# Kernel optimization log

Measured on AMD Instinct MI355X. Metric: run time of the kernel, lower is better.

The kernel has to match this reference:

```python
import jax, jax.numpy as jnp
import numpy as np

IN_F, OUT_F = 4096, 14336
F8_MAX = 448.0  # max magnitude of float8_e4m3fn


def setup_inputs() -> dict:
    key = jax.random.key(0)
    kx, kw, kb = jax.random.split(key, 3)
    x = jax.random.normal(kx, (2, 512, IN_F), dtype=jnp.bfloat16)
    w = jax.random.normal(kw, (OUT_F, IN_F), dtype=jnp.float32) * 0.02
    # per-tensor scale: amax / 448 (as in F8Linear.__init__)
    w_scale = (jnp.maximum(jnp.abs(w).max(), 1e-30) / F8_MAX).astype(jnp.float32)
    # quantize to fp8 e4m3; roundtrip back to float32 so the stored values are
    # exactly the fp8-representable values (float32 container keeps the bwd
    # reference's jax.vjp happy while the math is identical)
    w_f8 = jnp.clip(w / w_scale, -F8_MAX, F8_MAX).astype(jnp.float8_e4m3fn).astype(jnp.float32)
    bias = jax.random.normal(kb, (OUT_F,), dtype=jnp.float32) * 0.02
    return {"x": x, "weight_f8": w_f8, "w_scale": w_scale, "bias": bias}


def reference(x, weight_f8, w_scale, bias):
    # dequantize to activation dtype, then GEMM: y = x @ w^T + b
    w = weight_f8.astype(x.dtype) * w_scale.astype(x.dtype)   # [out, in]
    y = jnp.einsum('bsi,oi->bso', x, w) + bias.astype(x.dtype)
    return y
```

## Files before the change

### kernel.cpp

```cpp
#include <hip/hip_runtime.h>
#include <hip/hip_bf16.h>
#include <stdint.h>


#define IN_F   4096
#define OUT_F  14336
#define M_TOT  1024

#define BM 128
#define BN 128

#define TM 256
#define TN 256
#define TK 64
#define KT8 (IN_F / TK)

typedef __bf16  bf16x8 __attribute__((ext_vector_type(8)));
typedef __bf16  bf16x4 __attribute__((ext_vector_type(4)));
typedef float   f32x4  __attribute__((ext_vector_type(4)));

__device__ __forceinline__ void async_copy16(const void* g, void* l) {
    __builtin_amdgcn_global_load_lds(
        (const __attribute__((address_space(1))) void*)g,
        (__attribute__((address_space(3))) void*)l,
        16, 0, 0);
}

__global__ void detect_x_dtype(const uint32_t* __restrict__ xb,
                               int* __restrict__ flag) {
    __shared__ int any_low;
    if (threadIdx.x == 0) any_low = 0;
    __syncthreads();
    uint32_t bad = 0;
    for (int i = threadIdx.x; i < 1024; i += 256) bad |= (xb[i] & 0xFFFFu);
    if (bad) atomicOr(&any_low, 1);
    __syncthreads();
    if (threadIdx.x == 0) *flag = (any_low == 0) ? 1 : 0;
}

__global__ __launch_bounds__(256) void cvt_x_kernel(
    const void* __restrict__ xraw, bf16x8* __restrict__ out,
    const int* __restrict__ flag) {
    const int f32w = (*flag != 0);
    const int i = blockIdx.x * 256 + threadIdx.x;
    if (f32w) {
        const f32x4* in = (const f32x4*)xraw;
        f32x4 a = in[2 * i];
        f32x4 b = in[2 * i + 1];
        bf16x8 o;
        o[0] = (__bf16)a[0]; o[1] = (__bf16)a[1];
        o[2] = (__bf16)a[2]; o[3] = (__bf16)a[3];
        o[4] = (__bf16)b[0]; o[5] = (__bf16)b[1];
        o[6] = (__bf16)b[2]; o[7] = (__bf16)b[3];
        out[i] = o;
    } else {
        out[i] = ((const bf16x8*)xraw)[i];
    }
}

__global__ __launch_bounds__(512, 2) void gemm_fused_1b(
    const __bf16* __restrict__ xb,
    const float*  __restrict__ wf,
    const float*  __restrict__ w_scale,
    const float*  __restrict__ bias,
    void*         __restrict__ yraw,
    const int*    __restrict__ flag_p)
{
    __shared__ __align__(16) __bf16 As[2][2][128 * TK];
    __shared__ __align__(16) __bf16 Bs[2][2][128 * TK];

    const int f32w = (*flag_p != 0);
    const int t    = threadIdx.x;
    const int lane = t & 63;
    const int wv   = t >> 6;
    const int wm   = wv >> 2;
    const int wn   = wv & 3;
    const int lidx = lane & 15;
    const int q    = lane >> 4;

    const int flat = blockIdx.x;
    const int xcd  = flat & 7;
    const int slot = flat >> 3;
    const int ni   = xcd * 7 + (slot >> 2);
    const int mi   = slot & 3;
    const int m0   = mi * TM;
    const int n0   = ni * TN;

    const float scale = w_scale[0];

    const __bf16* gA = xb + (size_t)m0 * IN_F;

    int srow[2], scgl[2];
    #pragma unroll
    for (int i = 0; i < 2; ++i) {
        const int s = i * 512 + t;
        srow[i] = s >> 3;
        scgl[i] = (s & 7) ^ (srow[i] & 7);
    }

    const float* gB0 = wf + (size_t)(n0 + srow[0]) * IN_F + scgl[0] * 8;
    const float* gB1 = wf + (size_t)(n0 + srow[1]) * IN_F + scgl[1] * 8;

    int aoff[4][2], boff[2][2];
    #pragma unroll
    for (int qm = 0; qm < 4; ++qm) {
        const int row = qm * 32 + wm * 16 + lidx;
        #pragma unroll
        for (int kg = 0; kg < 2; ++kg)
            aoff[qm][kg] = row * 128 + (((kg * 4 + q) ^ (row & 7)) * 16);
    }
    #pragma unroll
    for (int qn = 0; qn < 2; ++qn) {
        const int row = qn * 64 + wn * 16 + lidx;
        #pragma unroll
        for (int kg = 0; kg < 2; ++kg)
            boff[qn][kg] = row * 128 + (((kg * 4 + q) ^ (row & 7)) * 16);
    }

    const f32x4 zero4 = {0.f, 0.f, 0.f, 0.f};
    f32x4 acc[8][4];
    #pragma unroll
    for (int i = 0; i < 8; ++i)
        #pragma unroll
        for (int j = 0; j < 4; ++j)
            acc[i][j] = zero4;

    bf16x8 areg[4][2], breg[2][2];
    f32x4 Br0[4], Br1[4];

#define STAGE_A(tile, half, BI) do {                                          \
    __bf16* _dst = &As[(BI)][(half)][0];                                      \
    const __bf16* _src = gA + (size_t)(half) * 128 * IN_F + (tile) * TK;      \
    async_copy16(_src + (size_t)srow[0] * IN_F + scgl[0] * 8, _dst + t * 8);  \
    async_copy16(_src + (size_t)srow[1] * IN_F + scgl[1] * 8,                 \
                 _dst + (512 + t) * 8);                                       \
} while (0)

#define B_LOAD(tile, half, Rv) do {                                           \
    const float* _p0 = gB0 + (size_t)(half) * 128 * IN_F + (tile) * TK;       \
    const float* _p1 = gB1 + (size_t)(half) * 128 * IN_F + (tile) * TK;       \
    Rv[0] = *(const f32x4*)_p0;                                               \
    Rv[1] = *(const f32x4*)(_p0 + 4);                                         \
    Rv[2] = *(const f32x4*)_p1;                                               \
    Rv[3] = *(const f32x4*)(_p1 + 4);                                         \
} while (0)

#define B_WRITE(half, BI, Rv) do {                                            \
    __bf16* _d = &Bs[(BI)][(half)][0];                                        \
    bf16x8 _o;                                                                \
    _o[0] = (__bf16)Rv[0][0]; _o[1] = (__bf16)Rv[0][1];                       \
    _o[2] = (__bf16)Rv[0][2]; _o[3] = (__bf16)Rv[0][3];                       \
    _o[4] = (__bf16)Rv[1][0]; _o[5] = (__bf16)Rv[1][1];                       \
    _o[6] = (__bf16)Rv[1][2]; _o[7] = (__bf16)Rv[1][3];                       \
    *(bf16x8*)(_d + (size_t)t * 8) = _o;                                      \
    _o[0] = (__bf16)Rv[2][0]; _o[1] = (__bf16)Rv[2][1];                       \
    _o[2] = (__bf16)Rv[2][2]; _o[3] = (__bf16)Rv[2][3];                       \
    _o[4] = (__bf16)Rv[3][0]; _o[5] = (__bf16)Rv[3][1];                       \
    _o[6] = (__bf16)Rv[3][2]; _o[7] = (__bf16)Rv[3][3];                       \
    *(bf16x8*)(_d + (size_t)(512 + t) * 8) = _o;                              \
} while (0)

#define LOAD_A(base) do {                                                     \
    _Pragma("unroll")                                                         \
    for (int _qm = 0; _qm < 4; ++_qm) {                                       \
        areg[_qm][0] = *(const bf16x8*)((base) + aoff[_qm][0]);               \
        areg[_qm][1] = *(const bf16x8*)((base) + aoff[_qm][1]);               \
    }                                                                         \
} while (0)

#define LOAD_B(base) do {                                                     \
    _Pragma("unroll")                                                         \
    for (int _qn = 0; _qn < 2; ++_qn) {                                       \
        breg[_qn][0] = *(const bf16x8*)((base) + boff[_qn][0]);               \
        breg[_qn][1] = *(const bf16x8*)((base) + boff[_qn][1]);               \
    }                                                                         \
} while (0)

#define MFMA16(MO, NO) do {                                                   \
    _Pragma("unroll")                                                         \
    for (int _qm = 0; _qm < 4; ++_qm)                                         \
        _Pragma("unroll")                                                     \
        for (int _qn = 0; _qn < 2; ++_qn) {                                   \
            acc[(MO) + _qm][(NO) + _qn] =                                     \
                __builtin_amdgcn_mfma_f32_16x16x32_bf16(                      \
                    areg[_qm][0], breg[_qn][0], acc[(MO) + _qm][(NO) + _qn],  \
                    0, 0, 0);                                                 \
            acc[(MO) + _qm][(NO) + _qn] =                                     \
                __builtin_amdgcn_mfma_f32_16x16x32_bf16(                      \
                    areg[_qm][1], breg[_qn][1], acc[(MO) + _qm][(NO) + _qn],  \
                    0, 0, 0);                                                 \
        }                                                                     \
} while (0)

#define BARR()    do { __builtin_amdgcn_s_barrier();                          \
                       asm volatile("" ::: "memory"); } while (0)
#define LGKM0()   asm volatile("s_waitcnt lgkmcnt(0)" ::: "memory")
#define VMCNT0()  asm volatile("s_waitcnt vmcnt(0)" ::: "memory")

    B_LOAD(0, 0, Br0);
    B_LOAD(0, 1, Br1);
    STAGE_A(0, 0, 0);
    STAGE_A(0, 1, 0);
    VMCNT0();
    B_WRITE(0, 0, Br0);
    B_WRITE(1, 0, Br1);
    LGKM0();
    BARR();

#define TILE_BODY(kt, P, QI) do {                                             \
    const char* _a0 = (const char*)&As[(P)][0][0];                            \
    const char* _a1 = (const char*)&As[(P)][1][0];                            \
    const char* _b0 = (const char*)&Bs[(P)][0][0];                            \
    const char* _b1 = (const char*)&Bs[(P)][1][0];                            \
    if ((kt) + 1 < KT8) {                                                     \
        B_LOAD((kt) + 1, 0, Br0);                                             \
        B_LOAD((kt) + 1, 1, Br1);                                             \
        STAGE_A((kt) + 1, 0, QI);                                             \
        STAGE_A((kt) + 1, 1, QI);                                             \
    }                                                                         \
    LOAD_A(_a0);                                                              \
    LOAD_B(_b0);                                                              \
    MFMA16(0, 0);                                                             \
    LOAD_B(_b1);                                                              \
    MFMA16(0, 2);                                                             \
    LOAD_A(_a1);                                                              \
    MFMA16(4, 2);                                                             \
    LOAD_B(_b0);                                                              \
    MFMA16(4, 0);                                                             \
    VMCNT0();      \
    if ((kt) + 1 < KT8) {                                                     \
        B_WRITE(0, QI, Br0);                                                  \
        B_WRITE(1, QI, Br1);                                                  \
    }                                                                         \
    LGKM0();                   \
    BARR();                                                                   \
} while (0)

    for (int it = 0; it < KT8 / 2; ++it) {
        const int kte = 2 * it;
        TILE_BODY(kte,     0, 1);
        TILE_BODY(kte + 1, 1, 0);
    }

#undef TILE_BODY
#undef STAGE_A
#undef B_LOAD
#undef B_WRITE
#undef LOAD_A
#undef LOAD_B
#undef MFMA16
#undef BARR
#undef LGKM0
#undef VMCNT0

    float bv[4];
    #pragma unroll
    for (int nf = 0; nf < 4; ++nf)
        bv[nf] = bias[n0 + (nf >> 1) * 128 + (nf & 1) * 64 + wn * 16 + lidx];

    if (f32w) {
        float* yf = (float*)yraw;
        #pragma unroll
        for (int mf = 0; mf < 8; ++mf)
            #pragma unroll
            for (int r = 0; r < 4; ++r) {
                const int m = m0 + (mf >> 2) * 128 + (mf & 3) * 32 + wm * 16 + q * 4 + r;
                float* yp = yf + (size_t)m * OUT_F + n0 + wn * 16 + lidx;
                #pragma unroll
                for (int nf = 0; nf < 4; ++nf)
                    yp[(nf >> 1) * 128 + (nf & 1) * 64] =
                        acc[mf][nf][r] * scale + bv[nf];
            }
    } else {
        __bf16* yh = (__bf16*)yraw;
        #pragma unroll
        for (int mf = 0; mf < 8; ++mf)
            #pragma unroll
            for (int r = 0; r < 4; ++r) {
                const int m = m0 + (mf >> 2) * 128 + (mf & 3) * 32 + wm * 16 + q * 4 + r;
                __bf16* yp = yh + (size_t)m * OUT_F + n0 + wn * 16 + lidx;
                #pragma unroll
                for (int nf = 0; nf < 4; ++nf)
                    yp[(nf >> 1) * 128 + (nf & 1) * 64] =
                        (__bf16)(acc[mf][nf][r] * scale + bv[nf]);
            }
    }
}

__global__ __launch_bounds__(256) void f8linear_fallback(
    const void*  __restrict__ xraw,
    const float* __restrict__ wq,
    const float* __restrict__ w_scale,
    const float* __restrict__ bias,
    void*        __restrict__ yraw,
    const int*   __restrict__ flag_p)
{
    __shared__ __align__(16) __bf16 As[BM * 40];
    __shared__ __align__(16) __bf16 Bs[BN * 40];

    const int f32w = (*flag_p != 0);
    const int t    = threadIdx.x;
    const int lane = t & 63;
    const int wv   = t >> 6;
    const int wm   = wv >> 1;
    const int wn   = wv & 1;
    const int lidx = lane & 15;
    const int q    = lane >> 4;

    const int flat = blockIdx.x;
    const int xcd  = flat & 7;
    const int slot = flat >> 3;
    const int ni   = xcd * 14 + (slot >> 3);
    const int mi   = slot & 7;
    const int m0   = mi * BM;
    const int n0   = ni * BN;

    const float scale = w_scale[0];
    const float*  xf = (const float*)xraw;
    const __bf16* xh = (const __bf16*)xraw;

    const int af_row = t >> 3;
    const int af_col = (t & 7) * 4;
    int ah_row[2], ah_cg[2];
    #pragma unroll
    for (int i = 0; i < 2; ++i) {
        const int s = i * 256 + t;
        ah_row[i] = s >> 2;
        ah_cg[i]  = s & 3;
    }
    const int b_row = t >> 3;
    const int b_col = (t & 7) * 4;

    const f32x4 zero4 = {0.f, 0.f, 0.f, 0.f};
    f32x4 acc[4][4];
    #pragma unroll
    for (int i = 0; i < 4; ++i)
        #pragma unroll
        for (int j = 0; j < 4; ++j)
            acc[i][j] = zero4;

    f32x4  aregf[4];
    bf16x8 aregh[2];
    f32x4  breg[4];
    if (f32w) {
        #pragma unroll
        for (int i = 0; i < 4; ++i)
            aregf[i] = *reinterpret_cast<const f32x4*>(
                xf + (size_t)(m0 + af_row + i * 32) * IN_F + af_col);
    } else {
        #pragma unroll
        for (int i = 0; i < 2; ++i)
            aregh[i] = *reinterpret_cast<const bf16x8*>(
                xh + (size_t)(m0 + ah_row[i]) * IN_F + ah_cg[i] * 8);
    }
    #pragma unroll
    for (int i = 0; i < 4; ++i)
        breg[i] = *reinterpret_cast<const f32x4*>(
            wq + (size_t)(n0 + i * 32 + b_row) * IN_F + b_col);

    for (int kt = 0; kt < 128; ++kt) {
        const int k0 = kt * 32;
        if (f32w) {
            #pragma unroll
            for (int i = 0; i < 4; ++i) {
                bf16x4 pk;
                pk[0] = (__bf16)aregf[i][0];
                pk[1] = (__bf16)aregf[i][1];
                pk[2] = (__bf16)aregf[i][2];
                pk[3] = (__bf16)aregf[i][3];
                *reinterpret_cast<bf16x4*>(As + (af_row + i * 32) * 40 + af_col) = pk;
            }
        } else {
            #pragma unroll
            for (int i = 0; i < 2; ++i)
                *reinterpret_cast<bf16x8*>(As + ah_row[i] * 40 + ah_cg[i] * 8) = aregh[i];
        }
        #pragma unroll
        for (int i = 0; i < 4; ++i) {
            bf16x4 pk;
            pk[0] = (__bf16)breg[i][0];
            pk[1] = (__bf16)breg[i][1];
            pk[2] = (__bf16)breg[i][2];
            pk[3] = (__bf16)breg[i][3];
            *reinterpret_cast<bf16x4*>(Bs + (i * 32 + b_row) * 40 + b_col) = pk;
        }
        __syncthreads();
        if (kt + 1 < 128) {
            const int k1 = k0 + 32;
            if (f32w) {
                #pragma unroll
                for (int i = 0; i < 4; ++i)
                    aregf[i] = *reinterpret_cast<const f32x4*>(
                        xf + (size_t)(m0 + af_row + i * 32) * IN_F + k1 + af_col);
            } else {
                #pragma unroll
                for (int i = 0; i < 2; ++i)
                    aregh[i] = *reinterpret_cast<const bf16x8*>(
                        xh + (size_t)(m0 + ah_row[i]) * IN_F + k1 + ah_cg[i] * 8);
            }
            #pragma unroll
            for (int i = 0; i < 4; ++i)
                breg[i] = *reinterpret_cast<const f32x4*>(
                    wq + (size_t)(n0 + i * 32 + b_row) * IN_F + k1 + b_col);
        }
        bf16x8 afr[4], bfr[4];
        #pragma unroll
        for (int mt = 0; mt < 4; ++mt) {
            const int row = wm * 64 + mt * 16 + lidx;
            afr[mt] = *reinterpret_cast<const bf16x8*>(As + row * 40 + q * 8);
        }
        #pragma unroll
        for (int nt = 0; nt < 4; ++nt) {
            const int row = wn * 64 + nt * 16 + lidx;
            bfr[nt] = *reinterpret_cast<const bf16x8*>(Bs + row * 40 + q * 8);
        }
        #pragma unroll
        for (int mt = 0; mt < 4; ++mt)
            #pragma unroll
            for (int nt = 0; nt < 4; ++nt)
                acc[mt][nt] = __builtin_amdgcn_mfma_f32_16x16x32_bf16(
                    afr[mt], bfr[nt], acc[mt][nt], 0, 0, 0);
        __syncthreads();
    }

    float bv[4];
    #pragma unroll
    for (int nt = 0; nt < 4; ++nt)
        bv[nt] = bias[n0 + wn * 64 + nt * 16 + lidx];

    if (f32w) {
        float* yf = (float*)yraw;
        #pragma unroll
        for (int mt = 0; mt < 4; ++mt)
            #pragma unroll
            for (int r = 0; r < 4; ++r) {
                const int m = m0 + wm * 64 + mt * 16 + q * 4 + r;
                float* yp = yf + (size_t)m * OUT_F + n0 + wn * 64 + lidx;
                #pragma unroll
                for (int nt = 0; nt < 4; ++nt)
                    yp[nt * 16] = acc[mt][nt][r] * scale + bv[nt];
            }
    } else {
        __bf16* yh = (__bf16*)yraw;
        #pragma unroll
        for (int mt = 0; mt < 4; ++mt)
            #pragma unroll
            for (int r = 0; r < 4; ++r) {
                const int m = m0 + wm * 64 + mt * 16 + q * 4 + r;
                __bf16* yp = yh + (size_t)m * OUT_F + n0 + wn * 64 + lidx;
                #pragma unroll
                for (int nt = 0; nt < 4; ++nt)
                    yp[nt * 16] = (__bf16)(acc[mt][nt][r] * scale + bv[nt]);
            }
    }
}

extern "C" void kernel_launch(void* const* d_in, const int* in_sizes, int n_in,
                              void* d_out, int out_size, void* d_ws, size_t ws_size,
                              hipStream_t stream) {
    const void* px = nullptr; const void* pw = nullptr;
    const void* ps = nullptr; const void* pb = nullptr;
    for (int i = 0; i < n_in; ++i) {
        const long sz = in_sizes[i];
        if      (sz == (long)M_TOT * IN_F) px = d_in[i];
        else if (sz == (long)OUT_F * IN_F) pw = d_in[i];
        else if (sz == 1)                  ps = d_in[i];
        else if (sz == OUT_F)              pb = d_in[i];
    }
    if (!px) px = d_in[0];
    if (!pw) pw = d_in[1];
    if (!ps) ps = d_in[2];
    if (!pb) pb = d_in[3];

    const size_t X_BYTES  = (size_t)M_TOT * IN_F * 2;
    const size_t FLAG_OFF = X_BYTES;

    if (ws_size >= FLAG_OFF + 16) {
        __bf16* xbf  = (__bf16*)d_ws;
        int*    flag = (int*)((char*)d_ws + FLAG_OFF);

        const int grid8 = (M_TOT / TM) * (OUT_F / TN);

        detect_x_dtype<<<1, 256, 0, stream>>>((const uint32_t*)px, flag);
        cvt_x_kernel<<<2048, 256, 0, stream>>>(px, (bf16x8*)xbf, flag);
        gemm_fused_1b<<<grid8, 512, 0, stream>>>(
            xbf, (const float*)pw, (const float*)ps, (const float*)pb,
            d_out, flag);
    } else {
        int* flag = (int*)d_ws;
        const int grid = (M_TOT / BM) * (OUT_F / BN);
        detect_x_dtype<<<1, 256, 0, stream>>>((const uint32_t*)px, flag);
        f8linear_fallback<<<grid, 256, 0, stream>>>(
            px, (const float*)pw, (const float*)ps, (const float*)pb, d_out, flag);
    }
}
```

Baseline: 465.0 us.

## Switch GEMM inner loop from 16x16x32 to 32x32x16 bf16 MFMA tiles

Replaces the 16x16x32 bf16 MFMA micro-tiling with 32x32x16 MFMAs. Each wave now owns a 128x64 output region, covering two 32-row blocks per A half and two 32-column blocks from one B half. The LDS fragment offsets, the per-k-step load/MFMA interleave and the epilogue row/column mapping are rewritten to match the 32x32 accumulator layout. The aim is to cut LDS fragment reads per MFMA and raise MFMA throughput per instruction. In exchange the accumulators become larger f32x16 vectors, which raises register pressure, and the epilogue stores are now strided differently.

```diff
diff --git a/kernel.cpp b/kernel.cpp
--- a/kernel.cpp
+++ b/kernel.cpp
@@ -18,6 +18,7 @@
 typedef __bf16  bf16x8 __attribute__((ext_vector_type(8)));
 typedef __bf16  bf16x4 __attribute__((ext_vector_type(4)));
 typedef float   f32x4  __attribute__((ext_vector_type(4)));
+typedef float   f32x16 __attribute__((ext_vector_type(16)));
 
 __device__ __forceinline__ void async_copy16(const void* g, void* l) {
     __builtin_amdgcn_global_load_lds(
@@ -58,7 +59,7 @@
     }
 }
 
-__global__ __launch_bounds__(512, 2) void gemm_fused_1b(
+__global__ __launch_bounds__(512, 2) void gemm_fused_32(
     const __bf16* __restrict__ xb,
     const float*  __restrict__ wf,
     const float*  __restrict__ w_scale,
@@ -75,8 +76,8 @@
     const int wv   = t >> 6;
     const int wm   = wv >> 2;
     const int wn   = wv & 3;
-    const int lidx = lane & 15;
-    const int q    = lane >> 4;
+    const int l31  = lane & 31;
+    const int hi   = lane >> 5;
 
     const int flat = blockIdx.x;
     const int xcd  = flat & 7;
@@ -101,31 +102,32 @@
     const float* gB0 = wf + (size_t)(n0 + srow[0]) * IN_F + scgl[0] * 8;
     const float* gB1 = wf + (size_t)(n0 + srow[1]) * IN_F + scgl[1] * 8;
 
-    int aoff[4][2], boff[2][2];
-    #pragma unroll
-    for (int qm = 0; qm < 4; ++qm) {
-        const int row = qm * 32 + wm * 16 + lidx;
-        #pragma unroll
-        for (int kg = 0; kg < 2; ++kg)
-            aoff[qm][kg] = row * 128 + (((kg * 4 + q) ^ (row & 7)) * 16);
-    }
-    #pragma unroll
-    for (int qn = 0; qn < 2; ++qn) {
-        const int row = qn * 64 + wn * 16 + lidx;
-        #pragma unroll
-        for (int kg = 0; kg < 2; ++kg)
-            boff[qn][kg] = row * 128 + (((kg * 4 + q) ^ (row & 7)) * 16);
-    }
-
-    const f32x4 zero4 = {0.f, 0.f, 0.f, 0.f};
-    f32x4 acc[8][4];
-    #pragma unroll
-    for (int i = 0; i < 8; ++i)
-        #pragma unroll
-        for (int j = 0; j < 4; ++j)
-            acc[i][j] = zero4;
-
-    bf16x8 areg[4][2], breg[2][2];
+    int aoffL[2][4], boffL[2][4];
+    #pragma unroll
+    for (int m01 = 0; m01 < 2; ++m01) {
+        const int r = wm * 64 + m01 * 32 + l31;
+        #pragma unroll
+        for (int ks = 0; ks < 4; ++ks)
+            aoffL[m01][ks] = r * 128 + (((ks * 2 + hi) ^ (r & 7)) * 16);
+    }
+    #pragma unroll
+    for (int nt = 0; nt < 2; ++nt) {
+        const int r = (wn & 1) * 64 + nt * 32 + l31;
+        #pragma unroll
+        for (int ks = 0; ks < 4; ++ks)
+            boffL[nt][ks] = r * 128 + (((ks * 2 + hi) ^ (r & 7)) * 16);
+    }
+    const int bhalf = wn >> 1;
+
+    const f32x16 zero16 = {0.f,0.f,0.f,0.f, 0.f,0.f,0.f,0.f,
+                           0.f,0.f,0.f,0.f, 0.f,0.f,0.f,0.f};
+    f32x16 acc[4][2];
+    #pragma unroll
+    for (int i = 0; i < 4; ++i) {
+        acc[i][0] = zero16;
+        acc[i][1] = zero16;
+    }
+
     f32x4 Br0[4], Br1[4];
 
 #define STAGE_A(tile, half, BI) do {                                          \
@@ -160,36 +162,21 @@
     *(bf16x8*)(_d + (size_t)(512 + t) * 8) = _o;                              \
 } while (0)
 
-#define LOAD_A(base) do {                                                     \
-    _Pragma("unroll")                                                         \
-    for (int _qm = 0; _qm < 4; ++_qm) {                                       \
-        areg[_qm][0] = *(const bf16x8*)((base) + aoff[_qm][0]);               \
-        areg[_qm][1] = *(const bf16x8*)((base) + aoff[_qm][1]);               \
-    }                                                                         \
-} while (0)
-
-#define LOAD_B(base) do {                                                     \
-    _Pragma("unroll")                                                         \
-    for (int _qn = 0; _qn < 2; ++_qn) {                                       \
-        breg[_qn][0] = *(const bf16x8*)((base) + boff[_qn][0]);               \
-        breg[_qn][1] = *(const bf16x8*)((base) + boff[_qn][1]);               \
-    }                                                                         \
-} while (0)
-
-#define MFMA16(MO, NO) do {                                                   \
-    _Pragma("unroll")                                                         \
-    for (int _qm = 0; _qm < 4; ++_qm)                                         \
-        _Pragma("unroll")                                                     \
-        for (int _qn = 0; _qn < 2; ++_qn) {                                   \
-            acc[(MO) + _qm][(NO) + _qn] =                                     \
-                __builtin_amdgcn_mfma_f32_16x16x32_bf16(                      \
-                    areg[_qm][0], breg[_qn][0], acc[(MO) + _qm][(NO) + _qn],  \
-                    0, 0, 0);                                                 \
-            acc[(MO) + _qm][(NO) + _qn] =                                     \
-                __builtin_amdgcn_mfma_f32_16x16x32_bf16(                      \
-                    areg[_qm][1], breg[_qn][1], acc[(MO) + _qm][(NO) + _qn],  \
-                    0, 0, 0);                                                 \
-        }                                                                     \
+#define KSTEP(a0p, a1p, bbp, ks) do {                                         \
+    bf16x8 _ar0 = *(const bf16x8*)((a0p) + aoffL[0][ks]);                     \
+    bf16x8 _ar1 = *(const bf16x8*)((a0p) + aoffL[1][ks]);                     \
+    bf16x8 _ar2 = *(const bf16x8*)((a1p) + aoffL[0][ks]);                     \
+    bf16x8 _ar3 = *(const bf16x8*)((a1p) + aoffL[1][ks]);                     \
+    bf16x8 _br0 = *(const bf16x8*)((bbp) + boffL[0][ks]);                     \
+    bf16x8 _br1 = *(const bf16x8*)((bbp) + boffL[1][ks]);                     \
+    acc[0][0] = __builtin_amdgcn_mfma_f32_32x32x16_bf16(_ar0, _br0, acc[0][0], 0, 0, 0); \
+    acc[0][1] = __builtin_amdgcn_mfma_f32_32x32x16_bf16(_ar0, _br1, acc[0][1], 0, 0, 0); \
+    acc[1][0] = __builtin_amdgcn_mfma_f32_32x32x16_bf16(_ar1, _br0, acc[1][0], 0, 0, 0); \
+    acc[1][1] = __builtin_amdgcn_mfma_f32_32x32x16_bf16(_ar1, _br1, acc[1][1], 0, 0, 0); \
+    acc[2][0] = __builtin_amdgcn_mfma_f32_32x32x16_bf16(_ar2, _br0, acc[2][0], 0, 0, 0); \
+    acc[2][1] = __builtin_amdgcn_mfma_f32_32x32x16_bf16(_ar2, _br1, acc[2][1], 0, 0, 0); \
+    acc[3][0] = __builtin_amdgcn_mfma_f32_32x32x16_bf16(_ar3, _br0, acc[3][0], 0, 0, 0); \
+    acc[3][1] = __builtin_amdgcn_mfma_f32_32x32x16_bf16(_ar3, _br1, acc[3][1], 0, 0, 0); \
 } while (0)
 
 #define BARR()    do { __builtin_amdgcn_s_barrier();                          \
@@ -210,23 +197,17 @@
 #define TILE_BODY(kt, P, QI) do {                                             \
     const char* _a0 = (const char*)&As[(P)][0][0];                            \
     const char* _a1 = (const char*)&As[(P)][1][0];                            \
-    const char* _b0 = (const char*)&Bs[(P)][0][0];                            \
-    const char* _b1 = (const char*)&Bs[(P)][1][0];                            \
+    const char* _bb = (const char*)&Bs[(P)][bhalf][0];                        \
     if ((kt) + 1 < KT8) {                                                     \
         B_LOAD((kt) + 1, 0, Br0);                                             \
         B_LOAD((kt) + 1, 1, Br1);                                             \
         STAGE_A((kt) + 1, 0, QI);                                             \
         STAGE_A((kt) + 1, 1, QI);                                             \
     }                                                                         \
-    LOAD_A(_a0);                                                              \
-    LOAD_B(_b0);                                                              \
-    MFMA16(0, 0);                                                             \
-    LOAD_B(_b1);                                                              \
-    MFMA16(0, 2);                                                             \
-    LOAD_A(_a1);                                                              \
-    MFMA16(4, 2);                                                             \
-    LOAD_B(_b0);                                                              \
-    MFMA16(4, 0);                                                             \
+    KSTEP(_a0, _a1, _bb, 0);                                                  \
+    KSTEP(_a0, _a1, _bb, 1);                                                  \
+    KSTEP(_a0, _a1, _bb, 2);                                                  \
+    KSTEP(_a0, _a1, _bb, 3);                                                  \
     VMCNT0();      \
     if ((kt) + 1 < KT8) {                                                     \
         B_WRITE(0, QI, Br0);                                                  \
@@ -246,44 +227,42 @@
 #undef STAGE_A
 #undef B_LOAD
 #undef B_WRITE
-#undef LOAD_A
-#undef LOAD_B
-#undef MFMA16
+#undef KSTEP
 #undef BARR
 #undef LGKM0
 #undef VMCNT0
 
-    float bv[4];
-    #pragma unroll
-    for (int nf = 0; nf < 4; ++nf)
-        bv[nf] = bias[n0 + (nf >> 1) * 128 + (nf & 1) * 64 + wn * 16 + lidx];
+    const int colbase = n0 + (wn >> 1) * 128 + (wn & 1) * 64 + l31;
+    float bv[2];
+    bv[0] = bias[colbase];
+    bv[1] = bias[colbase + 32];
 
     if (f32w) {
         float* yf = (float*)yraw;
         #pragma unroll
-        for (int mf = 0; mf < 8; ++mf)
-            #pragma unroll
-            for (int r = 0; r < 4; ++r) {
-                const int m = m0 + (mf >> 2) * 128 + (mf & 3) * 32 + wm * 16 + q * 4 + r;
-                float* yp = yf + (size_t)m * OUT_F + n0 + wn * 16 + lidx;
-                #pragma unroll
-                for (int nf = 0; nf < 4; ++nf)
-                    yp[(nf >> 1) * 128 + (nf & 1) * 64] =
-                        acc[mf][nf][r] * scale + bv[nf];
-            }
+        for (int mt = 0; mt < 4; ++mt) {
+            const int rowbase = m0 + (mt >> 1) * 128 + wm * 64 + (mt & 1) * 32 + 4 * hi;
+            #pragma unroll
+            for (int r = 0; r < 16; ++r) {
+                const int grow = rowbase + (r & 3) + 8 * (r >> 2);
+                float* yp = yf + (size_t)grow * OUT_F + colbase;
+                yp[0]  = acc[mt][0][r] * scale + bv[0];
+                yp[32] = acc[mt][1][r] * scale + bv[1];
+            }
+        }
     } else {
         __bf16* yh = (__bf16*)yraw;
         #pragma unroll
-        for (int mf = 0; mf < 8; ++mf)
-            #pragma unroll
-            for (int r = 0; r < 4; ++r) {
-                const int m = m0 + (mf >> 2) * 128 + (mf & 3) * 32 + wm * 16 + q * 4 + r;
-                __bf16* yp = yh + (size_t)m * OUT_F + n0 + wn * 16 + lidx;
-                #pragma unroll
-                for (int nf = 0; nf < 4; ++nf)
-                    yp[(nf >> 1) * 128 + (nf & 1) * 64] =
-                        (__bf16)(acc[mf][nf][r] * scale + bv[nf]);
-            }
+        for (int mt = 0; mt < 4; ++mt) {
+            const int rowbase = m0 + (mt >> 1) * 128 + wm * 64 + (mt & 1) * 32 + 4 * hi;
+            #pragma unroll
+            for (int r = 0; r < 16; ++r) {
+                const int grow = rowbase + (r & 3) + 8 * (r >> 2);
+                __bf16* yp = yh + (size_t)grow * OUT_F + colbase;
+                yp[0]  = (__bf16)(acc[mt][0][r] * scale + bv[0]);
+                yp[32] = (__bf16)(acc[mt][1][r] * scale + bv[1]);
+            }
+        }
     }
 }
 
@@ -483,7 +462,7 @@
 
         detect_x_dtype<<<1, 256, 0, stream>>>((const uint32_t*)px, flag);
         cvt_x_kernel<<<2048, 256, 0, stream>>>(px, (bf16x8*)xbf, flag);
-        gemm_fused_1b<<<grid8, 512, 0, stream>>>(
+        gemm_fused_32<<<grid8, 512, 0, stream>>>(
             xbf, (const float*)pw, (const float*)ps, (const float*)pb,
             d_out, flag);
     } else {
```

After: 456.5 us. No clear change (-1.8%).
